# Kernel tuning notes

Hardware: AMD Instinct MI355X
Metric: run time of the kernel (lower is better)

Reference implementation:

```python
import jax, jax.numpy as jnp
import numpy as np

B, L, E, H = 4, 2048, 1024, 16
D = E // H  # head_dim = 64

def setup_inputs() -> dict:
    key = jax.random.key(0)
    ks = jax.random.split(key, 8)
    s = 1.0 / np.sqrt(E)
    return {
        "x_q": jax.random.normal(ks[0], (B, L, E), jnp.float32),
        "x_k": jax.random.normal(ks[1], (B, L, E), jnp.float32),
        "x_v": jax.random.normal(ks[2], (B, L, E), jnp.float32),
        "Wq": jax.random.uniform(ks[3], (E, E), jnp.float32, -s, s),
        "Wk": jax.random.uniform(ks[4], (E, E), jnp.float32, -s, s),
        "Wv": jax.random.uniform(ks[5], (E, E), jnp.float32, -s, s),
        "Wo": jax.random.uniform(ks[6], (E, E), jnp.float32, -s, s),
        "bo": jax.random.uniform(ks[7], (E,), jnp.float32, -s, s),
    }

def reference(x_q, x_k, x_v, Wq, Wk, Wv, Wo, bo):
    # projections (torch Linear: y = x @ W.T)
    Q = (x_q @ Wq.T).reshape(B, L, H, D).transpose(0, 2, 1, 3)  # (B,H,Lq,D)
    K = (x_k @ Wk.T).reshape(B, L, H, D).transpose(0, 2, 1, 3)
    V = (x_v @ Wv.T).reshape(B, L, H, D).transpose(0, 2, 1, 3)
    scale = 1.0 / jnp.sqrt(jnp.asarray(D, Q.dtype))
    scores = jnp.einsum('bhqd,bhkd->bhqk', Q, K) * scale  # (B,H,Lq,Lk)
    attn = jax.nn.softmax(scores, axis=-1)
    ctx = jnp.einsum('bhqk,bhkd->bhqd', attn, V)
    ctx = ctx.transpose(0, 2, 1, 3).reshape(B, L, E)
    return ctx @ Wo.T + bo
```

## Files before the change

kernel.cpp:

```cpp
#include <hip/hip_runtime.h>
#include <hip/hip_bf16.h>
#include <stdint.h>

typedef __bf16 bf16;
typedef __attribute__((ext_vector_type(8))) __bf16 bf16x8;
typedef __attribute__((ext_vector_type(4))) __bf16 bf16x4;
typedef __attribute__((ext_vector_type(4))) float f32x4;
typedef __attribute__((ext_vector_type(16))) float f32x16;
typedef __attribute__((ext_vector_type(4))) unsigned int u32x4;

#define MFMA(a, b, c) __builtin_amdgcn_mfma_f32_16x16x32_bf16(a, b, c, 0, 0, 0)
#define MFMA32(a, b, c) __builtin_amdgcn_mfma_f32_32x32x16_bf16(a, b, c, 0, 0, 0)

__device__ __forceinline__ void gload16(const void* g, void* l) {
  __builtin_amdgcn_global_load_lds(
      (const __attribute__((address_space(1))) void*)g,
      (__attribute__((address_space(3))) void*)l, 16, 0, 0);
}

__global__ void cvt4(const float* __restrict__ s0, const float* __restrict__ s1,
                     const float* __restrict__ s2, const float* __restrict__ s3,
                     bf16* __restrict__ d0, bf16* __restrict__ d1,
                     bf16* __restrict__ d2, bf16* __restrict__ d3, long n) {
  const float* s = blockIdx.y == 0 ? s0 : blockIdx.y == 1 ? s1 : blockIdx.y == 2 ? s2 : s3;
  bf16* d       = blockIdx.y == 0 ? d0 : blockIdx.y == 1 ? d1 : blockIdx.y == 2 ? d2 : d3;
  long i0 = ((long)blockIdx.x * blockDim.x + threadIdx.x) * 8;
  long gs = (long)gridDim.x * blockDim.x * 8;
  for (long i = i0; i < n; i += gs) {
    float4 a = *(const float4*)(s + i);
    float4 b = *(const float4*)(s + i + 4);
    bf16x8 ov;
    ov[0] = (bf16)a.x; ov[1] = (bf16)a.y; ov[2] = (bf16)a.z; ov[3] = (bf16)a.w;
    ov[4] = (bf16)b.x; ov[5] = (bf16)b.y; ov[6] = (bf16)b.z; ov[7] = (bf16)b.w;
    *(bf16x8*)(d + i) = ov;
  }
}

__global__ __launch_bounds__(256) void gemm_bt(const bf16* __restrict__ A,
                                               const bf16* __restrict__ W,
                                               void* __restrict__ Cout,
                                               const float* __restrict__ bias,
                                               float scale, int mode) {
  __shared__ bf16 As[128 * 64];
  __shared__ bf16 Bs[128 * 64];
  const int tid = threadIdx.x;
  const int l = tid & 63, w = tid >> 6;
  const int lr = l & 15, lg = l >> 4;
  const int lin = blockIdx.y * 8 + blockIdx.x;
  const int nl = (lin & 7) * 64 + (lin >> 3);
  const int m0 = (nl >> 3) * 128, n0 = (nl & 7) * 128;
  const int wm = w >> 1, wn = w & 1;
  f32x4 acc[4][4];
  for (int i = 0; i < 4; i++)
    for (int j = 0; j < 4; j++)
      for (int r = 0; r < 4; r++) acc[i][j][r] = 0.f;

  const int srow = tid >> 3;
  const int schunk = tid & 7;

  for (int kt = 0; kt < 1024; kt += 64) {
#pragma unroll
    for (int i = 0; i < 4; i++) {
      int ar = i * 32 + srow;
      int ac = schunk ^ (ar & 7);
      gload16(A + (long)(m0 + ar) * 1024 + kt + ac * 8, (char*)As + i * 4096 + tid * 16);
      gload16(W + (long)(n0 + ar) * 1024 + kt + ac * 8, (char*)Bs + i * 4096 + tid * 16);
    }
    __syncthreads();
#pragma unroll
    for (int h = 0; h < 2; h++) {
      bf16x8 af[4], bw[4];
#pragma unroll
      for (int i = 0; i < 4; i++) {
        int row = wm * 64 + i * 16 + lr;
        af[i] = *(const bf16x8*)((const char*)As + row * 128 + (((h * 4 + lg) ^ (lr & 7)) << 4));
      }
#pragma unroll
      for (int j = 0; j < 4; j++) {
        int row = wn * 64 + j * 16 + lr;
        bw[j] = *(const bf16x8*)((const char*)Bs + row * 128 + (((h * 4 + lg) ^ (lr & 7)) << 4));
      }
#pragma unroll
      for (int i = 0; i < 4; i++)
#pragma unroll
        for (int j = 0; j < 4; j++)
          acc[i][j] = MFMA(af[i], bw[j], acc[i][j]);
    }
    __syncthreads();
  }

  for (int i = 0; i < 4; i++)
    for (int j = 0; j < 4; j++) {
      int row = m0 + wm * 64 + i * 16 + lg * 4;
      int col = n0 + wn * 64 + j * 16 + lr;
      f32x4 v = acc[i][j];
      if (mode == 2) {
        float* O = (float*)Cout;
        float bb = bias[col];
        for (int r = 0; r < 4; r++) O[(long)(row + r) * 1024 + col] = v[r] + bb;
      } else if (mode == 0) {
        bf16* O = (bf16*)Cout;
        for (int r = 0; r < 4; r++) {
          int rr = row + r;
          long idx = ((long)((rr >> 11) * 16 + (col >> 6)) * 2048 + (rr & 2047)) * 64 + (col & 63);
          O[idx] = (bf16)(v[r] * scale);
        }
      } else {
        bf16* O = (bf16*)Cout;
        long idx = ((long)((row >> 11) * 16 + (col >> 6)) * 64 + (col & 63)) * 2048 + (row & 2047);
        bf16x4 pk;
        for (int r = 0; r < 4; r++) pk[r] = (bf16)v[r];
        *(bf16x4*)(O + idx) = pk;
      }
    }
}

__global__ __launch_bounds__(512, 4) void attn_fwd(const bf16* __restrict__ Q,
                                                   const bf16* __restrict__ K,
                                                   const bf16* __restrict__ Vt,
                                                   bf16* __restrict__ ctx) {
  __shared__ bf16 Ks[2][128 * 64];
  __shared__ bf16 Vs[2][64 * 128];
  const int tid = threadIdx.x;
  const int l = tid & 63, w = tid >> 6;
  const int q32 = l & 31, hl = l >> 5;
  const int lin = blockIdx.y * 8 + blockIdx.x;
  const int nl = (lin & 7) * 64 + (lin >> 3);
  const int bh = nl >> 3, qt = nl & 7;
  const bf16* Qh = Q + (long)bh * 2048 * 64;
  const bf16* Kh = K + (long)bh * 2048 * 64;
  const bf16* Vh = Vt + (long)bh * 64 * 2048;
  const int qb = qt * 256 + w * 32;

#define STAGE(kv0, buf)                                                          \
  {                                                                              \
    _Pragma("unroll") for (int i = 0; i < 2; i++) {                              \
      int c = i * 512 + tid;                                                     \
      int kr = c >> 3, kc = c & 7;                                               \
      gload16(Kh + (long)((kv0) + kr) * 64 + ((kc ^ (kr & 7)) << 3),             \
              (char*)Ks[buf] + c * 16);                                          \
    }                                                                            \
    _Pragma("unroll") for (int i = 0; i < 2; i++) {                              \
      int c = i * 512 + tid;                                                     \
      int vr = c >> 4, vc = c & 15;                                              \
      int vsw = (vc & 8) | ((vc & 7) ^ (vr & 7));                                \
      gload16(Vh + (long)vr * 2048 + (kv0) + vsw * 8,                            \
              (char*)Vs[buf] + c * 16);                                          \
    }                                                                            \
  }

  bf16x8 bq[4];
#pragma unroll
  for (int kk = 0; kk < 4; kk++)
    bq[kk] = *(const bf16x8*)(Qh + (long)(qb + q32) * 64 + kk * 16 + hl * 8);

  f32x16 o0, o1;
#pragma unroll
  for (int r = 0; r < 16; r++) { o0[r] = 0.f; o1[r] = 0.f; }
  float lrun = 0.f;

  STAGE(0, 0);
  __syncthreads();

  for (int t = 0; t < 16; t++) {
    const int cur = t & 1;
    if (t < 15) STAGE((t + 1) * 128, cur ^ 1);
    const bf16* Kc = Ks[cur];
    const bf16* Vc = Vs[cur];
    f32x4 psum = {0.f, 0.f, 0.f, 0.f};

#pragma unroll
    for (int nn = 0; nn < 4; nn++) {
      const int row = nn * 32 + q32;
      f32x16 acc;
#pragma unroll
      for (int r = 0; r < 16; r++) acc[r] = 0.f;
      __builtin_amdgcn_s_setprio(1);
#pragma unroll
      for (int kk = 0; kk < 4; kk++) {
        int ch = (kk * 2 + hl) ^ (row & 7);
        bf16x8 ak = *(const bf16x8*)((const char*)Kc + row * 128 + (ch << 4));
        acc = MFMA32(ak, bq[kk], acc);
      }
      __builtin_amdgcn_s_setprio(0);

      f32x16 p;
#pragma unroll
      for (int r = 0; r < 16; r++) p[r] = __builtin_amdgcn_exp2f(acc[r]);
      f32x4 t4;
#pragma unroll
      for (int j = 0; j < 4; j++) t4[j] = (p[j] + p[4 + j]) + (p[8 + j] + p[12 + j]);
      psum += t4;

      unsigned wd[8];
#pragma unroll
      for (int i = 0; i < 8; i++) {
        float lo = p[2 * i], hi = p[2 * i + 1];
        asm("v_cvt_pk_bf16_f32 %0, %1, %2" : "=v"(wd[i]) : "v"(lo), "v"(hi));
      }
#pragma unroll
      for (int ss = 0; ss < 2; ss++) {
        unsigned a0 = wd[ss * 4 + 0], b0 = wd[ss * 4 + 2];
        unsigned a1 = wd[ss * 4 + 1], b1 = wd[ss * 4 + 3];
        asm("v_permlane32_swap_b32 %0, %1" : "+v"(a0), "+v"(b0));
        asm("v_permlane32_swap_b32 %0, %1" : "+v"(a1), "+v"(b1));
        u32x4 pw = {a0, a1, b0, b1};
        bf16x8 bp = *(bf16x8*)&pw;
        int ch0 = (nn * 2 + ss) * 2 + hl;
        __builtin_amdgcn_s_setprio(1);
#pragma unroll
        for (int nd = 0; nd < 2; nd++) {
          int vrw = nd * 32 + q32;
          int ch = (ch0 & 8) | ((ch0 & 7) ^ (vrw & 7));
          bf16x8 av = *(const bf16x8*)((const char*)Vc + vrw * 256 + (ch << 4));
          if (nd == 0) o0 = MFMA32(av, bp, o0);
          else         o1 = MFMA32(av, bp, o1);
        }
        __builtin_amdgcn_s_setprio(0);
      }
    }
    lrun += (psum[0] + psum[1]) + (psum[2] + psum[3]);
    __syncthreads();
  }

  lrun += __shfl_xor(lrun, 32);
  const int b = bh >> 4, h = bh & 15;
  const float inv = 1.0f / lrun;
  const int q = qb + q32;
#pragma unroll
  for (int nd = 0; nd < 2; nd++)
#pragma unroll
    for (int qd = 0; qd < 4; qd++) {
      bf16x4 pk;
#pragma unroll
      for (int r = 0; r < 4; r++)
        pk[r] = (bf16)((nd == 0 ? o0[qd * 4 + r] : o1[qd * 4 + r]) * inv);
      int d = nd * 32 + qd * 8 + hl * 4;
      *(bf16x4*)(ctx + ((long)b * 2048 + q) * 1024 + h * 64 + d) = pk;
    }
#undef STAGE
}

extern "C" void kernel_launch(void* const* d_in, const int* in_sizes, int n_in,
                              void* d_out, int out_size, void* d_ws, size_t ws_size,
                              hipStream_t stream) {
  const float* xq = (const float*)d_in[0];
  const float* xk = (const float*)d_in[1];
  const float* xv = (const float*)d_in[2];
  const float* Wq = (const float*)d_in[3];
  const float* Wk = (const float*)d_in[4];
  const float* Wv = (const float*)d_in[5];
  const float* Wo = (const float*)d_in[6];
  const float* bo = (const float*)d_in[7];

  char* p = (char*)d_ws;
  const size_t SZ_X = (size_t)8192 * 1024 * 2;
  const size_t SZ_W = (size_t)1024 * 1024 * 2;
  bf16* xqb = (bf16*)p; p += SZ_X;
  bf16* xkb = (bf16*)p; p += SZ_X;
  bf16* xvb = (bf16*)p; p += SZ_X;
  bf16* wqb = (bf16*)p; p += SZ_W;
  bf16* wkb = (bf16*)p; p += SZ_W;
  bf16* wvb = (bf16*)p; p += SZ_W;
  bf16* wob = (bf16*)p; p += SZ_W;
  bf16* Qb  = (bf16*)p; p += SZ_X;
  bf16* Kb  = (bf16*)p; p += SZ_X;
  bf16* Vtb = (bf16*)p; p += SZ_X;
  bf16* ctxb = (bf16*)p; p += SZ_X;
  (void)ws_size; (void)in_sizes; (void)n_in; (void)out_size;

  const float QSCALE = 0.18033688011112042f;

  cvt4<<<dim3(1024, 3), 256, 0, stream>>>(xq, xk, xv, xq, xqb, xkb, xvb, xqb,
                                          (long)8192 * 1024);
  cvt4<<<dim3(128, 4), 256, 0, stream>>>(Wq, Wk, Wv, Wo, wqb, wkb, wvb, wob,
                                         (long)1024 * 1024);
  gemm_bt<<<dim3(8, 64), 256, 0, stream>>>(xqb, wqb, Qb, nullptr, QSCALE, 0);
  gemm_bt<<<dim3(8, 64), 256, 0, stream>>>(xkb, wkb, Kb, nullptr, 1.0f, 0);
  gemm_bt<<<dim3(8, 64), 256, 0, stream>>>(xvb, wvb, Vtb, nullptr, 1.0f, 1);
  attn_fwd<<<dim3(8, 64), 512, 0, stream>>>(Qb, Kb, Vtb, ctxb);
  gemm_bt<<<dim3(8, 64), 256, 0, stream>>>(ctxb, wob, d_out, bo, 1.0f, 2);
}
```

Before: 205.0 us.

## Fuse fp32-to-bf16 activation conversion into batched QKV GEMM with double buffering

```diff
diff --git a/kernel.cpp b/kernel.cpp
--- a/kernel.cpp
+++ b/kernel.cpp
@@ -36,13 +36,13 @@
   }
 }
 
-__global__ __launch_bounds__(256) void gemm_bt(const bf16* __restrict__ A,
-                                               const bf16* __restrict__ W,
-                                               void* __restrict__ Cout,
-                                               const float* __restrict__ bias,
-                                               float scale, int mode) {
-  __shared__ bf16 As[128 * 64];
-  __shared__ bf16 Bs[128 * 64];
+template <int AF32>
+__device__ __forceinline__ void gemm_body(const void* __restrict__ Av,
+                                          const bf16* __restrict__ W,
+                                          void* __restrict__ Cout,
+                                          const float* __restrict__ bias,
+                                          float scale, int mode,
+                                          bf16* As, bf16* Bs) {
   const int tid = threadIdx.x;
   const int l = tid & 63, w = tid >> 6;
   const int lr = l & 15, lg = l >> 4;
@@ -50,6 +50,8 @@
   const int nl = (lin & 7) * 64 + (lin >> 3);
   const int m0 = (nl >> 3) * 128, n0 = (nl & 7) * 128;
   const int wm = w >> 1, wn = w & 1;
+  const bf16* A16 = (const bf16*)Av;
+  const float* A32 = (const float*)Av;
   f32x4 acc[4][4];
   for (int i = 0; i < 4; i++)
     for (int j = 0; j < 4; j++)
@@ -58,27 +60,71 @@
   const int srow = tid >> 3;
   const int schunk = tid & 7;
 
-  for (int kt = 0; kt < 1024; kt += 64) {
+  float4 areg[4][2];
+  auto ALOAD = [&](int kt) {
+#pragma unroll
+    for (int i = 0; i < 4; i++) {
+      int ar = i * 32 + srow;
+      const float* src = A32 + (long)(m0 + ar) * 1024 + kt + schunk * 8;
+      areg[i][0] = *(const float4*)(src);
+      areg[i][1] = *(const float4*)(src + 4);
+    }
+  };
+  auto AWRITE = [&](int buf) {
+#pragma unroll
+    for (int i = 0; i < 4; i++) {
+      int ar = i * 32 + srow;
+      bf16x8 v;
+      v[0] = (bf16)areg[i][0].x; v[1] = (bf16)areg[i][0].y;
+      v[2] = (bf16)areg[i][0].z; v[3] = (bf16)areg[i][0].w;
+      v[4] = (bf16)areg[i][1].x; v[5] = (bf16)areg[i][1].y;
+      v[6] = (bf16)areg[i][1].z; v[7] = (bf16)areg[i][1].w;
+      *(bf16x8*)((char*)As + buf * 16384 + ar * 128 + ((schunk ^ (ar & 7)) << 4)) = v;
+    }
+  };
+  auto WSTAGE = [&](int kt, int buf) {
 #pragma unroll
     for (int i = 0; i < 4; i++) {
       int ar = i * 32 + srow;
       int ac = schunk ^ (ar & 7);
-      gload16(A + (long)(m0 + ar) * 1024 + kt + ac * 8, (char*)As + i * 4096 + tid * 16);
-      gload16(W + (long)(n0 + ar) * 1024 + kt + ac * 8, (char*)Bs + i * 4096 + tid * 16);
-    }
-    __syncthreads();
+      gload16(W + (long)(n0 + ar) * 1024 + kt + ac * 8,
+              (char*)Bs + buf * 16384 + i * 4096 + tid * 16);
+    }
+  };
+  auto ASTAGE16 = [&](int kt, int buf) {
+#pragma unroll
+    for (int i = 0; i < 4; i++) {
+      int ar = i * 32 + srow;
+      int ac = schunk ^ (ar & 7);
+      gload16(A16 + (long)(m0 + ar) * 1024 + kt + ac * 8,
+              (char*)As + buf * 16384 + i * 4096 + tid * 16);
+    }
+  };
+
+  if (AF32) { ALOAD(0); WSTAGE(0, 0); AWRITE(0); }
+  else      { ASTAGE16(0, 0); WSTAGE(0, 0); }
+  __syncthreads();
+
+  for (int t = 0; t < 16; t++) {
+    const int cur = t & 1;
+    if (t < 15) {
+      if (AF32) { ALOAD((t + 1) * 64); WSTAGE((t + 1) * 64, cur ^ 1); }
+      else      { ASTAGE16((t + 1) * 64, cur ^ 1); WSTAGE((t + 1) * 64, cur ^ 1); }
+    }
+    const char* Ac = (const char*)As + cur * 16384;
+    const char* Bc = (const char*)Bs + cur * 16384;
 #pragma unroll
     for (int h = 0; h < 2; h++) {
       bf16x8 af[4], bw[4];
 #pragma unroll
       for (int i = 0; i < 4; i++) {
         int row = wm * 64 + i * 16 + lr;
-        af[i] = *(const bf16x8*)((const char*)As + row * 128 + (((h * 4 + lg) ^ (lr & 7)) << 4));
+        af[i] = *(const bf16x8*)(Ac + row * 128 + (((h * 4 + lg) ^ (lr & 7)) << 4));
       }
 #pragma unroll
       for (int j = 0; j < 4; j++) {
         int row = wn * 64 + j * 16 + lr;
-        bw[j] = *(const bf16x8*)((const char*)Bs + row * 128 + (((h * 4 + lg) ^ (lr & 7)) << 4));
+        bw[j] = *(const bf16x8*)(Bc + row * 128 + (((h * 4 + lg) ^ (lr & 7)) << 4));
       }
 #pragma unroll
       for (int i = 0; i < 4; i++)
@@ -86,6 +132,7 @@
         for (int j = 0; j < 4; j++)
           acc[i][j] = MFMA(af[i], bw[j], acc[i][j]);
     }
+    if (AF32 && t < 15) AWRITE(cur ^ 1);
     __syncthreads();
   }
 
@@ -115,6 +162,32 @@
     }
 }
 
+__global__ __launch_bounds__(256) void gemm_qkv(const float* __restrict__ xq,
+                                                const float* __restrict__ xk,
+                                                const float* __restrict__ xv,
+                                                const bf16* __restrict__ Wb,
+                                                bf16* __restrict__ Ob,
+                                                float qscale) {
+  __shared__ bf16 As[2][128 * 64];
+  __shared__ bf16 Bs[2][128 * 64];
+  const int z = blockIdx.z;
+  const float* A = z == 0 ? xq : (z == 1 ? xk : xv);
+  const bf16* W = Wb + (long)z * 1024 * 1024;
+  bf16* O = Ob + (long)z * 8192 * 1024;
+  const float scale = (z == 0) ? qscale : 1.0f;
+  const int mode = (z == 2) ? 1 : 0;
+  gemm_body<1>(A, W, O, nullptr, scale, mode, &As[0][0], &Bs[0][0]);
+}
+
+__global__ __launch_bounds__(256) void gemm_out(const bf16* __restrict__ A,
+                                                const bf16* __restrict__ W,
+                                                float* __restrict__ Cout,
+                                                const float* __restrict__ bias) {
+  __shared__ bf16 As[2][128 * 64];
+  __shared__ bf16 Bs[2][128 * 64];
+  gemm_body<0>(A, W, Cout, bias, 1.0f, 2, &As[0][0], &Bs[0][0]);
+}
+
 __global__ __launch_bounds__(512, 4) void attn_fwd(const bf16* __restrict__ Q,
                                                    const bf16* __restrict__ K,
                                                    const bf16* __restrict__ Vt,
@@ -142,9 +215,9 @@
     }                                                                            \
     _Pragma("unroll") for (int i = 0; i < 2; i++) {                              \
       int c = i * 512 + tid;                                                     \
-      int vr = c >> 4, vc = c & 15;                                              \
-      int vsw = (vc & 8) | ((vc & 7) ^ (vr & 7));                                \
-      gload16(Vh + (long)vr * 2048 + (kv0) + vsw * 8,                            \
+      int r = c >> 4, v0 = c & 15;                                               \
+      int vc = (v0 & 8) | ((v0 & 7) ^ (r & 7));                                  \
+      gload16(Vh + (long)r * 2048 + (kv0) + vc * 8,                              \
               (char*)Vs[buf] + c * 16);                                          \
     }                                                                            \
   }
@@ -256,9 +329,6 @@
   char* p = (char*)d_ws;
   const size_t SZ_X = (size_t)8192 * 1024 * 2;
   const size_t SZ_W = (size_t)1024 * 1024 * 2;
-  bf16* xqb = (bf16*)p; p += SZ_X;
-  bf16* xkb = (bf16*)p; p += SZ_X;
-  bf16* xvb = (bf16*)p; p += SZ_X;
   bf16* wqb = (bf16*)p; p += SZ_W;
   bf16* wkb = (bf16*)p; p += SZ_W;
   bf16* wvb = (bf16*)p; p += SZ_W;
@@ -271,13 +341,9 @@
 
   const float QSCALE = 0.18033688011112042f;
 
-  cvt4<<<dim3(1024, 3), 256, 0, stream>>>(xq, xk, xv, xq, xqb, xkb, xvb, xqb,
-                                          (long)8192 * 1024);
   cvt4<<<dim3(128, 4), 256, 0, stream>>>(Wq, Wk, Wv, Wo, wqb, wkb, wvb, wob,
                                          (long)1024 * 1024);
-  gemm_bt<<<dim3(8, 64), 256, 0, stream>>>(xqb, wqb, Qb, nullptr, QSCALE, 0);
-  gemm_bt<<<dim3(8, 64), 256, 0, stream>>>(xkb, wkb, Kb, nullptr, 1.0f, 0);
-  gemm_bt<<<dim3(8, 64), 256, 0, stream>>>(xvb, wvb, Vtb, nullptr, 1.0f, 1);
+  gemm_qkv<<<dim3(8, 64, 3), 256, 0, stream>>>(xq, xk, xv, wqb, Qb, QSCALE);
   attn_fwd<<<dim3(8, 64), 512, 0, stream>>>(Qb, Kb, Vtb, ctxb);
-  gemm_bt<<<dim3(8, 64), 256, 0, stream>>>(ctxb, wob, d_out, bo, 1.0f, 2);
-}
+  gemm_out<<<dim3(8, 64), 256, 0, stream>>>(ctxb, wob, (float*)d_out, bo);
+}
```

Result: faster. 197.1 us (-3.9%).

## Pipeline GEMM with 4-stage LDS ring and batch QKV projections into one launch

Applied to the files above, without the earlier changes.

```diff
diff --git a/kernel.cpp b/kernel.cpp
--- a/kernel.cpp
+++ b/kernel.cpp
@@ -36,13 +36,12 @@
   }
 }
 
-__global__ __launch_bounds__(256) void gemm_bt(const bf16* __restrict__ A,
-                                               const bf16* __restrict__ W,
-                                               void* __restrict__ Cout,
-                                               const float* __restrict__ bias,
-                                               float scale, int mode) {
-  __shared__ bf16 As[128 * 64];
-  __shared__ bf16 Bs[128 * 64];
+__device__ __forceinline__ void gemm_body(const bf16* __restrict__ A,
+                                          const bf16* __restrict__ W,
+                                          void* __restrict__ Cout,
+                                          const float* __restrict__ bias,
+                                          float scale, int mode,
+                                          bf16* As, bf16* Bs) {
   const int tid = threadIdx.x;
   const int l = tid & 63, w = tid >> 6;
   const int lr = l & 15, lg = l >> 4;
@@ -55,38 +54,44 @@
     for (int j = 0; j < 4; j++)
       for (int r = 0; r < 4; r++) acc[i][j][r] = 0.f;
 
-  const int srow = tid >> 3;
-  const int schunk = tid & 7;
-
-  for (int kt = 0; kt < 1024; kt += 64) {
+  auto STAGE = [&](int kt, int buf) {
+#pragma unroll
+    for (int i = 0; i < 2; i++) {
+      int c = i * 256 + tid;
+      int row = c >> 2, ch = c & 3;
+      int sc = (ch ^ ((row >> 1) & 3)) * 8;
+      gload16(A + (long)(m0 + row) * 1024 + kt + sc, (char*)As + buf * 8192 + c * 16);
+      gload16(W + (long)(n0 + row) * 1024 + kt + sc, (char*)Bs + buf * 8192 + c * 16);
+    }
+  };
+
+  STAGE(0, 0); STAGE(32, 1); STAGE(64, 2);
+
+  for (int t = 0; t < 32; t++) {
+    if (t <= 29)      asm volatile("s_waitcnt vmcnt(8) lgkmcnt(0)" ::: "memory");
+    else if (t == 30) asm volatile("s_waitcnt vmcnt(4) lgkmcnt(0)" ::: "memory");
+    else              asm volatile("s_waitcnt vmcnt(0) lgkmcnt(0)" ::: "memory");
+    __builtin_amdgcn_s_barrier();
+    __builtin_amdgcn_sched_barrier(0);
+    const char* Ac = (const char*)As + (t & 3) * 8192;
+    const char* Bc = (const char*)Bs + (t & 3) * 8192;
+    bf16x8 af[4], bw[4];
 #pragma unroll
     for (int i = 0; i < 4; i++) {
-      int ar = i * 32 + srow;
-      int ac = schunk ^ (ar & 7);
-      gload16(A + (long)(m0 + ar) * 1024 + kt + ac * 8, (char*)As + i * 4096 + tid * 16);
-      gload16(W + (long)(n0 + ar) * 1024 + kt + ac * 8, (char*)Bs + i * 4096 + tid * 16);
-    }
-    __syncthreads();
-#pragma unroll
-    for (int h = 0; h < 2; h++) {
-      bf16x8 af[4], bw[4];
-#pragma unroll
-      for (int i = 0; i < 4; i++) {
-        int row = wm * 64 + i * 16 + lr;
-        af[i] = *(const bf16x8*)((const char*)As + row * 128 + (((h * 4 + lg) ^ (lr & 7)) << 4));
-      }
-#pragma unroll
-      for (int j = 0; j < 4; j++) {
-        int row = wn * 64 + j * 16 + lr;
-        bw[j] = *(const bf16x8*)((const char*)Bs + row * 128 + (((h * 4 + lg) ^ (lr & 7)) << 4));
-      }
-#pragma unroll
-      for (int i = 0; i < 4; i++)
-#pragma unroll
-        for (int j = 0; j < 4; j++)
-          acc[i][j] = MFMA(af[i], bw[j], acc[i][j]);
-    }
-    __syncthreads();
+      int row = wm * 64 + i * 16 + lr;
+      af[i] = *(const bf16x8*)(Ac + row * 64 + ((lg ^ ((row >> 1) & 3)) << 4));
+    }
+#pragma unroll
+    for (int j = 0; j < 4; j++) {
+      int row = wn * 64 + j * 16 + lr;
+      bw[j] = *(const bf16x8*)(Bc + row * 64 + ((lg ^ ((row >> 1) & 3)) << 4));
+    }
+#pragma unroll
+    for (int i = 0; i < 4; i++)
+#pragma unroll
+      for (int j = 0; j < 4; j++)
+        acc[i][j] = MFMA(af[i], bw[j], acc[i][j]);
+    if (t <= 28) STAGE((t + 3) * 32, (t + 3) & 3);
   }
 
   for (int i = 0; i < 4; i++)
@@ -115,6 +120,30 @@
     }
 }
 
+__global__ __launch_bounds__(256) void gemm_qkv(const bf16* __restrict__ Xb,
+                                                const bf16* __restrict__ Wb,
+                                                bf16* __restrict__ Ob,
+                                                float qscale) {
+  __shared__ bf16 As[4][128 * 32];
+  __shared__ bf16 Bs[4][128 * 32];
+  const int z = blockIdx.z;
+  const bf16* A = Xb + (long)z * 8192 * 1024;
+  const bf16* W = Wb + (long)z * 1024 * 1024;
+  bf16* O = Ob + (long)z * 8192 * 1024;
+  const float scale = (z == 0) ? qscale : 1.0f;
+  const int mode = (z == 2) ? 1 : 0;
+  gemm_body(A, W, O, nullptr, scale, mode, &As[0][0], &Bs[0][0]);
+}
+
+__global__ __launch_bounds__(256) void gemm_out(const bf16* __restrict__ A,
+                                                const bf16* __restrict__ W,
+                                                float* __restrict__ Cout,
+                                                const float* __restrict__ bias) {
+  __shared__ bf16 As[4][128 * 32];
+  __shared__ bf16 Bs[4][128 * 32];
+  gemm_body(A, W, Cout, bias, 1.0f, 2, &As[0][0], &Bs[0][0]);
+}
+
 __global__ __launch_bounds__(512, 4) void attn_fwd(const bf16* __restrict__ Q,
                                                    const bf16* __restrict__ K,
                                                    const bf16* __restrict__ Vt,
@@ -142,9 +171,9 @@
     }                                                                            \
     _Pragma("unroll") for (int i = 0; i < 2; i++) {                              \
       int c = i * 512 + tid;                                                     \
-      int vr = c >> 4, vc = c & 15;                                              \
-      int vsw = (vc & 8) | ((vc & 7) ^ (vr & 7));                                \
-      gload16(Vh + (long)vr * 2048 + (kv0) + vsw * 8,                            \
+      int r = c >> 4, v0 = c & 15;                                               \
+      int vc = (v0 & 8) | ((v0 & 7) ^ (r & 7));                                  \
+      gload16(Vh + (long)r * 2048 + (kv0) + vc * 8,                              \
               (char*)Vs[buf] + c * 16);                                          \
     }                                                                            \
   }
@@ -275,9 +304,7 @@
                                           (long)8192 * 1024);
   cvt4<<<dim3(128, 4), 256, 0, stream>>>(Wq, Wk, Wv, Wo, wqb, wkb, wvb, wob,
                                          (long)1024 * 1024);
-  gemm_bt<<<dim3(8, 64), 256, 0, stream>>>(xqb, wqb, Qb, nullptr, QSCALE, 0);
-  gemm_bt<<<dim3(8, 64), 256, 0, stream>>>(xkb, wkb, Kb, nullptr, 1.0f, 0);
-  gemm_bt<<<dim3(8, 64), 256, 0, stream>>>(xvb, wvb, Vtb, nullptr, 1.0f, 1);
+  gemm_qkv<<<dim3(8, 64, 3), 256, 0, stream>>>(xqb, wqb, Qb, QSCALE);
   attn_fwd<<<dim3(8, 64), 512, 0, stream>>>(Qb, Kb, Vtb, ctxb);
-  gemm_bt<<<dim3(8, 64), 256, 0, stream>>>(ctxb, wob, d_out, bo, 1.0f, 2);
-}
+  gemm_out<<<dim3(8, 64), 256, 0, stream>>>(ctxb, wob, (float*)d_out, bo);
+}
```

After: 200.6 us. 1.02x faster.
